# Performance work log

Measured on AMD Instinct MI355X. Metric: run time of the kernel, lower is better.

## Reference

```python
import jax, jax.numpy as jnp
import numpy as np

B = 512; S = 6; Q = 2            # meta-batch, n_way*k_shot, n_way*q_query
DIM = 64; IMG = 28; N_WAY = 2
HEADS = 4; HD = DIM // HEADS     # retrieval heads / head dim
EPS = 1e-5


def _pool_mat(inp, out):
    # exact torch AdaptiveAvgPool2d windowing as a matrix [out, inp]
    P = np.zeros((out, inp), np.float32)
    for i in range(out):
        s = (i * inp) // out
        e = -((-(i + 1) * inp) // out)
        P[i, s:e] = 1.0 / (e - s)
    return jnp.asarray(P)

P28 = _pool_mat(IMG, 8)  # 28 -> 8; subsequent 8 -> 8 pools are identity


def _gelu(x):
    return jax.nn.gelu(x, approximate=False)


def _conv(x, w, b):
    y = jax.lax.conv_general_dilated(x, w, (1, 1), ((1, 1), (1, 1)),
                                     dimension_numbers=('NCHW', 'OIHW', 'NCHW'))
    return y + b[None, :, None, None]


def _bn(x, p):
    # p rows: gamma, beta, running_mean, running_var (eval-mode BatchNorm2d)
    g, bt, m, v = p[0], p[1], p[2], p[3]
    sc = g / jnp.sqrt(v + EPS)
    return (x - m[None, :, None, None]) * sc[None, :, None, None] + bt[None, :, None, None]


def _img_in(x, c1w, c1b, bn1, c2w, c2b, bn2, c3w, c3b, bn3, c4w, c4b, bn4, lin_w):
    h = _bn(_conv(x, c1w, c1b), bn1)
    h = jnp.einsum('oi,ncij,pj->ncop', P28, h, P28)   # adaptive avg pool 28x28 -> 8x8
    h = _gelu(h)                                       # dropout is identity in eval
    h = _gelu(_bn(_conv(h, c2w, c2b), bn2))
    h = _gelu(_bn(_conv(h, c3w, c3b), bn3))
    h = _gelu(_bn(_conv(h, c4w, c4b), bn4))            # -> [N,1,8,8]
    h = h.reshape(h.shape[0], -1)                      # [N,64]
    return h @ lin_w.T                                 # Linear(64 -> DIM, no bias)


def _net(x, w1, w2):
    # x: [B,K,D]; w1,w2: [B,D,D] batched fast weights
    h = jnp.einsum('bed,bkd->bke', w1, x)
    ah = _gelu(h)
    y = jnp.einsum('bed,bkd->bke', w2, ah)
    return y, h


def _get_lor(x, w1, w2, r_q, r_k, r_v, r_o, ln_w, ln_b):
    b, k, _ = x.shape
    q, _ = _net(x, w1, w2)
    qh = jnp.einsum('nhd,bkd->bknh', r_q, q)
    sc = jnp.einsum('bknh,rnh->bknr', qh, r_k) / (HD ** 0.5)
    p = jax.nn.softmax(sc, axis=-1)
    lor = jnp.einsum('bknr,rnh->bknh', p, r_v).reshape(b, k, DIM)
    lor = jnp.einsum('de,bkd->bke', r_o, lor)
    z = lor + x
    mu = z.mean(-1, keepdims=True)
    var = ((z - mu) ** 2).mean(-1, keepdims=True)
    return (z - mu) / jnp.sqrt(var + EPS) * ln_w + ln_b


def _forward(query_w, sxs, qxs, inner_lr, c1w, c1b, bn1, c2w, c2b, bn2, c3w, c3b, bn3,
             c4w, c4b, bn4, lin_w, emb, w1, w2, tags, r_q, r_k, r_v, r_o, ln_w, ln_b,
             sys, qys):
    b = query_w.shape[0]
    s = sxs.shape[1]
    q = qxs.shape[1]
    feats = lambda im: _img_in(im.reshape(-1, 1, IMG, IMG), c1w, c1b, bn1, c2w, c2b,
                               bn2, c3w, c3b, bn3, c4w, c4b, bn4, lin_w)
    sx = feats(sxs).reshape(b, s, DIM)
    qx = feats(qxs).reshape(b, q, DIM)
    qe = tags[4]
    w1b = jnp.broadcast_to(w1, (b, DIM, DIM))
    w2b = jnp.broadcast_to(w2, (b, DIM, DIM))
    bound = sx + emb[sys]                                          # [B,S,D]
    # all 4 tag variants for all S shots in one vectorized get_lor call
    inp = (bound[:, :, None, :] + tags[:4][None, None]).reshape(b, s * 4, DIM)
    lors = _get_lor(inp, w1b, w2b, r_q, r_k, r_v, r_o, ln_w, ln_b).reshape(b, s, 4, DIM)
    l1s, r1s, l2s, r2s = lors[:, :, 0], lors[:, :, 1], lors[:, :, 2], lors[:, :, 3]
    qw1 = w1[None] + jnp.einsum('bsl,bsr->blr', l1s, r1s)
    qw2 = w2[None] + jnp.einsum('bsl,bsr->blr', l2s, r2s)
    preds, _ = _net(qx + qe, qw1, qw2)                             # [B,Q,D]
    logits = jnp.einsum('ld,bqd->bql', emb, preds).reshape(-1, N_WAY)
    labels = qys.reshape(-1)
    ls = jax.nn.log_softmax(logits)
    task_loss = -jnp.take_along_axis(ls, labels[:, None], axis=1).mean()
    n_correct = (jnp.argmax(logits, axis=1) == labels).sum()
    return task_loss, n_correct, b * q


def setup_inputs() -> dict:
    key = jax.random.key(0)
    ks = jax.random.split(key, 24)
    rn = lambda i, sh, sc=1.0: sc * jax.random.normal(ks[i], sh, jnp.float32)
    def bnp(i, c):
        k0, k1, k2 = jax.random.split(ks[i], 3)
        return jnp.stack([1.0 + 0.1 * jax.random.normal(k0, (c,)),
                          0.1 * jax.random.normal(k1, (c,)),
                          0.1 * jax.random.normal(k2, (c,)),
                          0.5 + jax.random.uniform(jax.random.fold_in(ks[i], 3), (c,))])
    return {
        'query_w': rn(0, (B, DIM)),
        'sxs': rn(1, (B, S, IMG * IMG)),
        'qxs': rn(2, (B, Q, IMG * IMG)),
        'inner_lr': jnp.float32(0.1),
        'c1w': rn(3, (32, 1, 3, 3), 0.3), 'c1b': rn(4, (32,), 0.1), 'bn1': bnp(5, 32),
        'c2w': rn(6, (32, 32, 3, 3), 0.06), 'c2b': rn(7, (32,), 0.1), 'bn2': bnp(8, 32),
        'c3w': rn(9, (32, 32, 3, 3), 0.06), 'c3b': rn(10, (32,), 0.1), 'bn3': bnp(11, 32),
        'c4w': rn(12, (1, 32, 3, 3), 0.06), 'c4b': rn(13, (1,), 0.1), 'bn4': bnp(14, 1),
        'lin_w': rn(15, (DIM, 64), 0.125),
        'emb': rn(16, (N_WAY, DIM), 0.125),
        'w1': rn(17, (DIM, DIM), 0.125),
        'w2': rn(18, (DIM, DIM), 0.125),
        'tags': rn(19, (8, DIM), 0.125),
        'r_q': rn(20, (HEADS, HD, DIM), 0.125),
        'r_k': rn(21, (16, HEADS, HD), 0.25),
        'r_v': rn(22, (16, HEADS, HD), 0.25),
        'r_o': rn(23, (DIM, DIM), 0.125),
        'ln_w': 0.001 * jnp.ones((DIM,), jnp.float32),
        'ln_b': jnp.zeros((DIM,), jnp.float32),
        'sys': jax.random.randint(jax.random.fold_in(key, 100), (B, S), 0, N_WAY),
        'qys': jax.random.randint(jax.random.fold_in(key, 101), (B, Q), 0, N_WAY),
    }


def reference(query_w, sxs, qxs, inner_lr, c1w, c1b, bn1, c2w, c2b, bn2, c3w, c3b, bn3,
              c4w, c4b, bn4, lin_w, emb, w1, w2, tags, r_q, r_k, r_v, r_o, ln_w, ln_b,
              sys, qys):
    task_loss, n_correct, n_q = _forward(query_w, sxs, qxs, inner_lr, c1w, c1b, bn1,
                                         c2w, c2b, bn2, c3w, c3b, bn3, c4w, c4b, bn4,
                                         lin_w, emb, w1, w2, tags, r_q, r_k, r_v, r_o,
                                         ln_w, ln_b, sys, qys)
    return (task_loss, task_loss, jnp.float32(0.0), n_correct, n_q)
```

## Files before the change

kernel.cpp:

```cpp
#include <hip/hip_runtime.h>
#include <math.h>

constexpr int NSUP = 3072;
constexpr float EPSF = 1e-5f;

constexpr int WS_W1B  = 0;
constexpr int WS_B1   = 1024;
constexpr int WS_W2B  = 1056;
constexpr int WS_W3B  = 5664;
constexpr int WS_W4B  = 10272;
constexpr int WS_B4   = 10416;
constexpr int WS_B2   = 10420;
constexpr int WS_B3   = 10452;
constexpr int WS_HW1  = 10484;
constexpr int WS_HW2  = 12788;
constexpr int WS_HRQ  = 15092;
constexpr int WS_HROT = 17396;
constexpr int WS_PART = 19700;
constexpr int WS_FEATS= 20724;

using short8 = __attribute__((ext_vector_type(8))) short;
using f32x4  = __attribute__((ext_vector_type(4))) float;

__device__ __forceinline__ float gelu_f(float x) {
    float z  = fabsf(x) * 0.70710678118654752440f;
    float t  = __builtin_amdgcn_rcpf(__builtin_fmaf(0.3275911f, z, 1.0f));
    float p  = t * __builtin_fmaf(t,
                 __builtin_fmaf(t,
                   __builtin_fmaf(t,
                     __builtin_fmaf(t, 1.061405429f, -1.453152027f),
                     1.421413741f),
                   -0.284496736f),
                 0.254829592f);
    float e  = __expf(-z * z);
    float er = __builtin_fmaf(-p, e, 1.0f);
    float s  = copysignf(er, x);
    return 0.5f * x * (1.0f + s);
}
__device__ __forceinline__ unsigned short f2bf(float f) {
    unsigned u = __float_as_uint(f);
    return (unsigned short)((u + 0x7FFFu + ((u >> 16) & 1u)) >> 16);
}
__device__ __forceinline__ float bflo(unsigned u) { return __uint_as_float(u << 16); }
__device__ __forceinline__ float bfhi(unsigned u) { return __uint_as_float(u & 0xffff0000u); }

__global__ void __launch_bounds__(256) precompute_kernel(
    const float* __restrict__ c1w, const float* __restrict__ c1b, const float* __restrict__ bn1,
    const float* __restrict__ c2w, const float* __restrict__ c2b, const float* __restrict__ bn2,
    const float* __restrict__ c3w, const float* __restrict__ c3b, const float* __restrict__ bn3,
    const float* __restrict__ c4w, const float* __restrict__ c4b, const float* __restrict__ bn4,
    const float* __restrict__ w1, const float* __restrict__ w2,
    const float* __restrict__ rq, const float* __restrict__ ro,
    float* __restrict__ ws)
{
    const int gid = blockIdx.x * 256 + threadIdx.x;
    const int gsz = gridDim.x * 256;

    unsigned short* w1b = (unsigned short*)(ws + WS_W1B);
    for (int v = gid; v < 2048; v += gsz) {
        int kt = v >> 10, rem = v & 1023, oc = rem >> 5, kk = rem & 31;
        int tap = kt * 32 + kk;
        unsigned short o = 0;
        if (tap < 36) {
            int tt = tap / 6, s = tap - tt * 6;
            float sum = 0.f;
            for (int di = 0; di < 3; ++di) {
                int a = tt - di; if (a < 0 || a > 3) continue;
                for (int dj = 0; dj < 3; ++dj) {
                    int bb = s - dj; if (bb < 0 || bb > 3) continue;
                    sum += c1w[oc * 9 + di * 3 + dj];
                }
            }
            float sc1 = bn1[oc] * rsqrtf(bn1[96 + oc] + EPSF);
            o = f2bf(sum * sc1 * (1.0f / 16.0f));
        }
        w1b[v] = o;
    }
    for (int c = gid; c < 32; c += gsz) {
        float sc1 = bn1[c] * rsqrtf(bn1[96 + c] + EPSF);
        ws[WS_B1 + c] = (c1b[c] - bn1[64 + c]) * sc1 + bn1[32 + c];
        float sc2 = bn2[c] * rsqrtf(bn2[96 + c] + EPSF);
        ws[WS_B2 + c] = (c2b[c] - bn2[64 + c]) * sc2 + bn2[32 + c];
        float sc3 = bn3[c] * rsqrtf(bn3[96 + c] + EPSF);
        ws[WS_B3 + c] = (c3b[c] - bn3[64 + c]) * sc3 + bn3[32 + c];
    }
    unsigned short* w2b = (unsigned short*)(ws + WS_W2B);
    unsigned short* w3b = (unsigned short*)(ws + WS_W3B);
    for (int v = gid; v < 9216; v += gsz) {
        int tap = v >> 10, oc = (v >> 5) & 31, ic = v & 31;
        float sc2 = bn2[oc] * rsqrtf(bn2[96 + oc] + EPSF);
        float sc3 = bn3[oc] * rsqrtf(bn3[96 + oc] + EPSF);
        w2b[v] = f2bf(c2w[oc * 288 + ic * 9 + tap] * sc2);
        w3b[v] = f2bf(c3w[oc * 288 + ic * 9 + tap] * sc3);
    }
    {
        unsigned short* w4b = (unsigned short*)(ws + WS_W4B);
        float sc4 = bn4[0] * rsqrtf(bn4[3] + EPSF);
        for (int v = gid; v < 288; v += gsz) {
            int tap = v >> 5, ic = v & 31;
            w4b[v] = f2bf(c4w[ic * 9 + tap] * sc4);
        }
        if (gid == 0) ws[WS_B4] = (c4b[0] - bn4[2]) * sc4 + bn4[1];
    }
    unsigned short* hw1 = (unsigned short*)(ws + WS_HW1);
    unsigned short* hw2 = (unsigned short*)(ws + WS_HW2);
    unsigned short* hrq = (unsigned short*)(ws + WS_HRQ);
    unsigned short* hro = (unsigned short*)(ws + WS_HROT);
    for (int v = gid; v < 4608; v += gsz) {
        int e = v / 72, d = v - e * 72;
        unsigned short a = 0, b = 0, c = 0, r = 0;
        if (d < 64) {
            a = f2bf(w1[e * 64 + d]);
            b = f2bf(w2[e * 64 + d]);
            c = f2bf(rq[e * 64 + d]);
            r = f2bf(ro[d * 64 + e]);
        }
        hw1[v] = a; hw2[v] = b; hrq[v] = c; hro[v] = r;
    }
}

__device__ __forceinline__ void conv32(unsigned short* __restrict__ A,
                                       const unsigned short* __restrict__ W,
                                       float bi0, float bi1, int col, int quad)
{
    f32x4 acc[4][2];
    #pragma unroll
    for (int mt = 0; mt < 4; ++mt) { acc[mt][0] = (f32x4){0,0,0,0}; acc[mt][1] = (f32x4){0,0,0,0}; }
    const unsigned short* abase[4];
    #pragma unroll
    for (int mt = 0; mt < 4; ++mt) {
        int px = mt * 16 + col;
        abase[mt] = A + ((px >> 3) * 10 + (px & 7)) * 32 + quad * 8;
    }
    #pragma unroll
    for (int dr = 0; dr < 3; ++dr)
        #pragma unroll
        for (int dc = 0; dc < 3; ++dc) {
            int tap = dr * 3 + dc;
            short8 b0 = *(const short8*)(W + (tap * 32 + col) * 32 + quad * 8);
            short8 b1 = *(const short8*)(W + (tap * 32 + 16 + col) * 32 + quad * 8);
            #pragma unroll
            for (int mt = 0; mt < 4; ++mt) {
                short8 a = *(const short8*)(abase[mt] + (dr * 10 + dc) * 32);
                acc[mt][0] = __builtin_amdgcn_mfma_f32_16x16x32_bf16(a, b0, acc[mt][0], 0, 0, 0);
                acc[mt][1] = __builtin_amdgcn_mfma_f32_16x16x32_bf16(a, b1, acc[mt][1], 0, 0, 0);
            }
        }
    #pragma unroll
    for (int mt = 0; mt < 4; ++mt)
        #pragma unroll
        for (int reg = 0; reg < 4; ++reg) {
            int px = mt * 16 + quad * 4 + reg;
            unsigned short* dst = A + (((px >> 3) + 1) * 10 + (px & 7) + 1) * 32;
            dst[col]      = f2bf(gelu_f(acc[mt][0][reg] + bi0));
            dst[col + 16] = f2bf(gelu_f(acc[mt][1][reg] + bi1));
        }
}

__global__ void __launch_bounds__(512, 4) feats_kernel(
    const float* __restrict__ sxs, const float* __restrict__ qxs,
    const float* __restrict__ lin_w, const float* __restrict__ ws,
    float* __restrict__ feats)
{
    __shared__ __align__(16) unsigned short sAct[8][3200];
    __shared__ __align__(16) unsigned short sWB[9216];
    __shared__ __align__(16) unsigned short sW4[288];
    __shared__ __align__(16) float sh4[8][64];

    const int t    = threadIdx.x;
    const int wv   = t >> 6;
    const int lane = t & 63;
    const int col  = lane & 15;
    const int quad = lane >> 4;
    const int n    = blockIdx.x * 8 + wv;

    unsigned short* A = sAct[wv];

    const uint4* w2v = (const uint4*)(ws + WS_W2B);
    uint4 pw0 = w2v[t];
    uint4 pw1 = w2v[t + 512];
    uint4 pw2 = {0, 0, 0, 0};
    if (t < 128) pw2 = w2v[t + 1024];

    {
        const float* img = (n < NSUP) ? (sxs + (size_t)n * 784) : (qxs + (size_t)(n - NSUP) * 784);
        const float4* sv = (const float4*)img;
        #pragma unroll
        for (int j = 0; j < 4; ++j) {
            int idx = j * 64 + lane;
            if (idx < 196) {
                float4 v = sv[idx];
                ushort4 o = { f2bf(v.x), f2bf(v.y), f2bf(v.z), f2bf(v.w) };
                *(ushort4*)(A + idx * 4) = o;
            }
        }
    }
    if (t < 256) ((uint4*)sWB)[t] = ((const uint4*)(ws + WS_W1B))[t];
    __syncthreads();

    {
        int ttj[8], ssj[8];
        #pragma unroll
        for (int j = 0; j < 8; ++j) {
            int k = quad * 8 + j;
            ttj[j] = k / 6; ssj[j] = k - ttj[j] * 6;
        }
        f32x4 acc[4][2];
        #pragma unroll
        for (int mt = 0; mt < 4; ++mt) { acc[mt][0] = (f32x4){0,0,0,0}; acc[mt][1] = (f32x4){0,0,0,0}; }

        short8 b00 = *(const short8*)(sWB + (0 * 32 + 0 * 16 + col) * 32 + quad * 8);
        short8 b01 = *(const short8*)(sWB + (0 * 32 + 1 * 16 + col) * 32 + quad * 8);
        short8 b10 = *(const short8*)(sWB + (1 * 32 + 0 * 16 + col) * 32 + quad * 8);
        short8 b11 = *(const short8*)(sWB + (1 * 32 + 1 * 16 + col) * 32 + quad * 8);

        #pragma unroll
        for (int mt = 0; mt < 4; ++mt) {
            int px = mt * 16 + col;
            int sr = (((px >> 3) * 7) >> 1) - 1;
            int sc = (((px & 7) * 7) >> 1) - 1;
            short8 a0;
            #pragma unroll
            for (int j = 0; j < 8; ++j) {
                int rr = sr + ttj[j], cc = sc + ssj[j];
                bool ok = ((unsigned)rr < 28u) && ((unsigned)cc < 28u);
                int off = ok ? (rr * 28 + cc) : 0;
                unsigned short hv = A[off];
                a0[j] = ok ? (short)hv : (short)0;
            }
            acc[mt][0] = __builtin_amdgcn_mfma_f32_16x16x32_bf16(a0, b00, acc[mt][0], 0, 0, 0);
            acc[mt][1] = __builtin_amdgcn_mfma_f32_16x16x32_bf16(a0, b01, acc[mt][1], 0, 0, 0);
            short8 a1 = {0,0,0,0,0,0,0,0};
            if (quad == 0) {
                #pragma unroll
                for (int j = 0; j < 4; ++j) {
                    int rr = sr + 5, cc = sc + 2 + j;
                    bool ok = ((unsigned)rr < 28u) && ((unsigned)cc < 28u);
                    int off = ok ? (rr * 28 + cc) : 0;
                    unsigned short hv = A[off];
                    a1[j] = ok ? (short)hv : (short)0;
                }
            }
            acc[mt][0] = __builtin_amdgcn_mfma_f32_16x16x32_bf16(a1, b10, acc[mt][0], 0, 0, 0);
            acc[mt][1] = __builtin_amdgcn_mfma_f32_16x16x32_bf16(a1, b11, acc[mt][1], 0, 0, 0);
        }

        {
            uint4 z4 = {0, 0, 0, 0};
            #pragma unroll
            for (int it = 0; it < 3; ++it) {
                int h = lane + it * 64;
                if (h < 144) {
                    int u4;
                    if (h < 40)      u4 = h;
                    else if (h < 80) u4 = 360 + (h - 40);
                    else {
                        int k = h - 80; int r = 1 + (k >> 3); int cj = k & 7;
                        u4 = r * 40 + ((cj >= 4) ? (32 + cj) : cj);
                    }
                    ((uint4*)A)[u4] = z4;
                }
            }
        }
        float bi0 = ws[WS_B1 + col], bi1 = ws[WS_B1 + 16 + col];
        #pragma unroll
        for (int mt = 0; mt < 4; ++mt)
            #pragma unroll
            for (int reg = 0; reg < 4; ++reg) {
                int px = mt * 16 + quad * 4 + reg;
                unsigned short* dst = A + (((px >> 3) + 1) * 10 + (px & 7) + 1) * 32;
                dst[col]      = f2bf(gelu_f(acc[mt][0][reg] + bi0));
                dst[col + 16] = f2bf(gelu_f(acc[mt][1][reg] + bi1));
            }
    }
    __syncthreads();

    {
        ((uint4*)sWB)[t]       = pw0;
        ((uint4*)sWB)[t + 512] = pw1;
        if (t < 128) ((uint4*)sWB)[t + 1024] = pw2;
        if (t < 36)  ((uint4*)sW4)[t] = ((const uint4*)(ws + WS_W4B))[t];
        const uint4* w3v = (const uint4*)(ws + WS_W3B);
        pw0 = w3v[t];
        pw1 = w3v[t + 512];
        if (t < 128) pw2 = w3v[t + 1024];
    }
    __syncthreads();

    conv32(A, sWB, ws[WS_B2 + col], ws[WS_B2 + 16 + col], col, quad);
    __syncthreads();
    {
        ((uint4*)sWB)[t]       = pw0;
        ((uint4*)sWB)[t + 512] = pw1;
        if (t < 128) ((uint4*)sWB)[t + 1024] = pw2;
    }
    __syncthreads();
    conv32(A, sWB, ws[WS_B3 + col], ws[WS_B3 + 16 + col], col, quad);

    {
        f32x4 acc4[4];
        #pragma unroll
        for (int mt = 0; mt < 4; ++mt) acc4[mt] = (f32x4){0,0,0,0};
        const unsigned short* abase[4];
        #pragma unroll
        for (int mt = 0; mt < 4; ++mt) {
            int px = mt * 16 + col;
            abase[mt] = A + ((px >> 3) * 10 + (px & 7)) * 32 + quad * 8;
        }
        #pragma unroll
        for (int dr = 0; dr < 3; ++dr)
            #pragma unroll
            for (int dc = 0; dc < 3; ++dc) {
                int tap = dr * 3 + dc;
                short8 b = *(const short8*)(sW4 + tap * 32 + quad * 8);
                #pragma unroll
                for (int mt = 0; mt < 4; ++mt) {
                    short8 a = *(const short8*)(abase[mt] + (dr * 10 + dc) * 32);
                    acc4[mt] = __builtin_amdgcn_mfma_f32_16x16x32_bf16(a, b, acc4[mt], 0, 0, 0);
                }
            }
        if (col < 4) {
            f32x4 v = acc4[0];
            if (col == 1) v = acc4[1];
            else if (col == 2) v = acc4[2];
            else if (col == 3) v = acc4[3];
            float b4 = ws[WS_B4];
            #pragma unroll
            for (int reg = 0; reg < 4; ++reg)
                sh4[wv][col * 16 + quad * 4 + reg] = gelu_f(v[reg] + b4);
        }
    }

    {
        const float4* lw = (const float4*)(lin_w + (size_t)lane * 64);
        const float4* hp = (const float4*)sh4[wv];
        float acc = 0.f;
        #pragma unroll
        for (int j = 0; j < 16; ++j) {
            float4 w = lw[j], h = hp[j];
            acc += w.x * h.x + w.y * h.y + w.z * h.z + w.w * h.w;
        }
        feats[n * 64 + lane] = acc;
    }
}

__device__ __forceinline__ void head_gemm(const unsigned short* __restrict__ Ab,
                                          const unsigned short* __restrict__ Bw,
                                          int col, int quad, int wvid, f32x4 res[2])
{
    #pragma unroll
    for (int u = 0; u < 2; ++u) {
        int tau = wvid + u * 4;
        int mt = tau & 1, nt = tau >> 1;
        f32x4 acc = {0, 0, 0, 0};
        #pragma unroll
        for (int kt = 0; kt < 2; ++kt) {
            short8 a = *(const short8*)(Ab + (mt * 16 + col) * 72 + kt * 32 + quad * 8);
            short8 b = *(const short8*)(Bw + (nt * 16 + col) * 72 + kt * 32 + quad * 8);
            acc = __builtin_amdgcn_mfma_f32_16x16x32_bf16(a, b, acc, 0, 0, 0);
        }
        res[u] = acc;
    }
}

__global__ void __launch_bounds__(256, 2) head_kernel(
    const float* __restrict__ emb, const float* __restrict__ tags,
    const float* __restrict__ rk, const float* __restrict__ rv,
    const float* __restrict__ lnw, const float* __restrict__ lnb,
    const int* __restrict__ sys, const int* __restrict__ qys,
    const float* __restrict__ ws, const float* __restrict__ feats,
    float* __restrict__ part)
{
    __shared__ __align__(16) unsigned short sW1B[4608], sW2B[4608], sRQB[4608], sROT[4608];
    __shared__ __align__(16) unsigned short bufA[2304], bufB[2304];
    __shared__ __align__(16) float sXf[1536];
    __shared__ __align__(16) float sRK[1024], sRV[1024];
    __shared__ __align__(16) float s_xq[128], s_ah[128], s_yp[128];
    __shared__ float s_t1[12], s_t2[12], s_mu[24], s_rs[24], s_lg[4];

    const int t    = threadIdx.x;
    const int b    = blockIdx.x;
    const int wvid = t >> 6;
    const int col  = t & 15;
    const int quad = (t >> 4) & 3;

    ((float4*)sRK)[t] = ((const float4*)rk)[t];
    ((float4*)sRV)[t] = ((const float4*)rv)[t];
    for (int i = t; i < 576; i += 256) {
        ((uint4*)sW1B)[i] = ((const uint4*)(ws + WS_HW1))[i];
        ((uint4*)sW2B)[i] = ((const uint4*)(ws + WS_HW2))[i];
        ((uint4*)sRQB)[i] = ((const uint4*)(ws + WS_HRQ))[i];
        ((uint4*)sROT)[i] = ((const uint4*)(ws + WS_HROT))[i];
    }
    if (t < 72) {
        uint4 z = {0, 0, 0, 0};
        ((uint4*)(bufA + 1728))[t] = z;
        ((uint4*)(bufB + 1728))[t] = z;
    }
    for (int idx = t; idx < 1536; idx += 256) {
        int k = idx >> 6, e = idx & 63;
        int s = k >> 2, tg = k & 3;
        int cls = sys[b * 6 + s];
        float v = feats[(b * 6 + s) * 64 + e] + emb[cls * 64 + e] + tags[tg * 64 + e];
        sXf[idx] = v;
        bufA[k * 72 + e] = f2bf(v);
    }
    __syncthreads();

    f32x4 r[2];
    head_gemm(bufA, sW1B, col, quad, wvid, r);
    #pragma unroll
    for (int u = 0; u < 2; ++u) {
        int tau = wvid + u * 4, mt = tau & 1, nt = tau >> 1;
        #pragma unroll
        for (int reg = 0; reg < 4; ++reg) {
            int row = mt * 16 + quad * 4 + reg;
            if (row < 24) bufB[row * 72 + nt * 16 + col] = f2bf(gelu_f(r[u][reg]));
        }
    }
    __syncthreads();
    head_gemm(bufB, sW2B, col, quad, wvid, r);
    #pragma unroll
    for (int u = 0; u < 2; ++u) {
        int tau = wvid + u * 4, mt = tau & 1, nt = tau >> 1;
        #pragma unroll
        for (int reg = 0; reg < 4; ++reg) {
            int row = mt * 16 + quad * 4 + reg;
            if (row < 24) bufA[row * 72 + nt * 16 + col] = f2bf(r[u][reg]);
        }
    }
    __syncthreads();
    head_gemm(bufA, sRQB, col, quad, wvid, r);
    #pragma unroll
    for (int u = 0; u < 2; ++u) {
        int tau = wvid + u * 4, mt = tau & 1, nt = tau >> 1;
        #pragma unroll
        for (int reg = 0; reg < 4; ++reg) {
            int row = mt * 16 + quad * 4 + reg;
            if (row < 24) bufB[row * 72 + nt * 16 + col] = f2bf(r[u][reg]);
        }
    }
    __syncthreads();

    if (t < 96) {
        int k = t >> 2, nn = t & 3;
        const unsigned short* qp = bufB + k * 72 + nn * 16;
        uint4 u0 = *(const uint4*)(qp);
        uint4 u1 = *(const uint4*)(qp + 8);
        float qv[16];
        qv[0]=bflo(u0.x); qv[1]=bfhi(u0.x); qv[2]=bflo(u0.y); qv[3]=bfhi(u0.y);
        qv[4]=bflo(u0.z); qv[5]=bfhi(u0.z); qv[6]=bflo(u0.w); qv[7]=bfhi(u0.w);
        qv[8]=bflo(u1.x); qv[9]=bfhi(u1.x); qv[10]=bflo(u1.y); qv[11]=bfhi(u1.y);
        qv[12]=bflo(u1.z); qv[13]=bfhi(u1.z); qv[14]=bflo(u1.w); qv[15]=bfhi(u1.w);
        float sc[16]; float mx = -1e30f;
        #pragma unroll
        for (int rr = 0; rr < 16; ++rr) {
            const float* kp = sRK + rr * 64 + nn * 16;
            float d = 0.f;
            #pragma unroll
            for (int h = 0; h < 16; ++h) d += qv[h] * kp[h];
            d *= 0.25f;
            sc[rr] = d; mx = fmaxf(mx, d);
        }
        float sum = 0.f;
        #pragma unroll
        for (int rr = 0; rr < 16; ++rr) { sc[rr] = __expf(sc[rr] - mx); sum += sc[rr]; }
        float inv = 1.0f / sum;
        float o[16];
        #pragma unroll
        for (int h = 0; h < 16; ++h) o[h] = 0.f;
        #pragma unroll
        for (int rr = 0; rr < 16; ++rr) {
            const float* vp = sRV + rr * 64 + nn * 16;
            float p = sc[rr];
            #pragma unroll
            for (int h = 0; h < 16; ++h) o[h] += p * vp[h];
        }
        unsigned short* op = bufA + k * 72 + nn * 16;
        #pragma unroll
        for (int h = 0; h < 16; ++h) op[h] = f2bf(o[h] * inv);
    }
    __syncthreads();

    head_gemm(bufA, sROT, col, quad, wvid, r);
    #pragma unroll
    for (int u = 0; u < 2; ++u) {
        int tau = wvid + u * 4, mt = tau & 1, nt = tau >> 1;
        #pragma unroll
        for (int reg = 0; reg < 4; ++reg) {
            int row = mt * 16 + quad * 4 + reg;
            if (row < 24) {
                int idx = row * 64 + nt * 16 + col;
                sXf[idx] = sXf[idx] + r[u][reg];
            }
        }
    }
    __syncthreads();

    if (t < 24) {
        const float4* zp = (const float4*)(sXf + t * 64);
        float sx_ = 0.f;
        #pragma unroll
        for (int j = 0; j < 16; ++j) {
            float4 v = zp[(j + t) & 15];
            sx_ += v.x + v.y + v.z + v.w;
        }
        float mu = sx_ * (1.0f / 64.0f);
        float vv = 0.f;
        #pragma unroll
        for (int j = 0; j < 16; ++j) {
            float4 v = zp[(j + t) & 15];
            float d0 = v.x - mu, d1 = v.y - mu, d2 = v.z - mu, d3 = v.w - mu;
            vv += d0*d0 + d1*d1 + d2*d2 + d3*d3;
        }
        s_mu[t] = mu;
        s_rs[t] = 1.0f / sqrtf(vv * (1.0f / 64.0f) + EPSF);
    }
    __syncthreads();
    for (int idx = t; idx < 1536; idx += 256) {
        int k = idx >> 6, e = idx & 63;
        float v = (sXf[idx] - s_mu[k]) * s_rs[k] * lnw[e] + lnb[e];
        bufB[k * 72 + e] = f2bf(v);
    }
    if (t < 128) {
        int q = t >> 6, e = t & 63;
        s_xq[t] = feats[(NSUP + b * 2 + q) * 64 + e] + tags[256 + e];
    }
    __syncthreads();

    if (t < 12) {
        int q = t / 6, s = t - q * 6;
        const uint4* rp = (const uint4*)(bufB + (s * 4 + 1) * 72);
        const float* xp = s_xq + q * 64;
        float d = 0.f;
        #pragma unroll
        for (int j = 0; j < 8; ++j) {
            uint4 u = rp[j];
            const float* x = xp + j * 8;
            d += bflo(u.x)*x[0] + bfhi(u.x)*x[1] + bflo(u.y)*x[2] + bfhi(u.y)*x[3]
               + bflo(u.z)*x[4] + bfhi(u.z)*x[5] + bflo(u.w)*x[6] + bfhi(u.w)*x[7];
        }
        s_t1[t] = d;
    }
    __syncthreads();
    if (t < 128) {
        int q = t >> 6, e = t & 63;
        const uint4* wp = (const uint4*)(sW1B + e * 72);
        const float* xp = s_xq + q * 64;
        float acc = 0.f;
        #pragma unroll
        for (int j = 0; j < 8; ++j) {
            uint4 u = wp[j];
            const float* x = xp + j * 8;
            acc += bflo(u.x)*x[0] + bfhi(u.x)*x[1] + bflo(u.y)*x[2] + bfhi(u.y)*x[3]
                 + bflo(u.z)*x[4] + bfhi(u.z)*x[5] + bflo(u.w)*x[6] + bfhi(u.w)*x[7];
        }
        #pragma unroll
        for (int s = 0; s < 6; ++s)
            acc += bflo((unsigned)bufB[(s * 4 + 0) * 72 + e]) * s_t1[q * 6 + s];
        s_ah[t] = gelu_f(acc);
    }
    __syncthreads();
    if (t < 12) {
        int q = t / 6, s = t - q * 6;
        const uint4* rp = (const uint4*)(bufB + (s * 4 + 3) * 72);
        const float* xp = s_ah + q * 64;
        float d = 0.f;
        #pragma unroll
        for (int j = 0; j < 8; ++j) {
            uint4 u = rp[j];
            const float* x = xp + j * 8;
            d += bflo(u.x)*x[0] + bfhi(u.x)*x[1] + bflo(u.y)*x[2] + bfhi(u.y)*x[3]
               + bflo(u.z)*x[4] + bfhi(u.z)*x[5] + bflo(u.w)*x[6] + bfhi(u.w)*x[7];
        }
        s_t2[t] = d;
    }
    __syncthreads();
    if (t < 128) {
        int q = t >> 6, e = t & 63;
        const uint4* wp = (const uint4*)(sW2B + e * 72);
        const float* xp = s_ah + q * 64;
        float acc = 0.f;
        #pragma unroll
        for (int j = 0; j < 8; ++j) {
            uint4 u = wp[j];
            const float* x = xp + j * 8;
            acc += bflo(u.x)*x[0] + bfhi(u.x)*x[1] + bflo(u.y)*x[2] + bfhi(u.y)*x[3]
                 + bflo(u.z)*x[4] + bfhi(u.z)*x[5] + bflo(u.w)*x[6] + bfhi(u.w)*x[7];
        }
        #pragma unroll
        for (int s = 0; s < 6; ++s)
            acc += bflo((unsigned)bufB[(s * 4 + 2) * 72 + e]) * s_t2[q * 6 + s];
        s_yp[t] = acc;
    }
    __syncthreads();
    if (t < 4) {
        int q = t >> 1, ll = t & 1;
        const float4* ep = (const float4*)(emb + ll * 64);
        const float4* yp = (const float4*)(s_yp + q * 64);
        float d = 0.f;
        #pragma unroll
        for (int j = 0; j < 16; ++j) {
            float4 a = ep[j], x = yp[j];
            d += a.x*x.x + a.y*x.y + a.z*x.z + a.w*x.w;
        }
        s_lg[t] = d;
    }
    __syncthreads();
    if (t == 0) {
        float lsum = 0.f, corr = 0.f;
        #pragma unroll
        for (int q = 0; q < 2; ++q) {
            float l0 = s_lg[q * 2], l1 = s_lg[q * 2 + 1];
            int lab = qys[b * 2 + q];
            float m = fmaxf(l0, l1);
            float lse = m + logf(expf(l0 - m) + expf(l1 - m));
            lsum += -((lab ? l1 : l0) - lse);
            int pred = (l1 > l0) ? 1 : 0;
            corr += (pred == lab) ? 1.0f : 0.0f;
        }
        part[b] = lsum;
        part[512 + b] = corr;
    }
}

__global__ void __launch_bounds__(256) finalize_kernel(const float* __restrict__ part,
                                                       float* __restrict__ out)
{
    __shared__ float sl[256], sc[256];
    const int t = threadIdx.x;
    sl[t] = part[t] + part[t + 256];
    sc[t] = part[512 + t] + part[768 + t];
    __syncthreads();
    for (int s = 128; s > 0; s >>= 1) {
        if (t < s) { sl[t] += sl[t + s]; sc[t] += sc[t + s]; }
        __syncthreads();
    }
    if (t == 0) {
        float loss = sl[0] * (1.0f / 1024.0f);
        out[0] = loss;
        out[1] = loss;
        out[2] = 0.0f;
        out[3] = sc[0];
        out[4] = 1024.0f;
    }
}

extern "C" void kernel_launch(void* const* d_in, const int* in_sizes, int n_in,
                              void* d_out, int out_size, void* d_ws, size_t ws_size,
                              hipStream_t stream)
{
    (void)in_sizes; (void)n_in; (void)out_size; (void)ws_size;
    const float* sxs  = (const float*)d_in[1];
    const float* qxs  = (const float*)d_in[2];
    const float* c1w  = (const float*)d_in[4];
    const float* c1b  = (const float*)d_in[5];
    const float* bn1  = (const float*)d_in[6];
    const float* c2w  = (const float*)d_in[7];
    const float* c2b  = (const float*)d_in[8];
    const float* bn2  = (const float*)d_in[9];
    const float* c3w  = (const float*)d_in[10];
    const float* c3b  = (const float*)d_in[11];
    const float* bn3  = (const float*)d_in[12];
    const float* c4w  = (const float*)d_in[13];
    const float* c4b  = (const float*)d_in[14];
    const float* bn4  = (const float*)d_in[15];
    const float* lin_w= (const float*)d_in[16];
    const float* emb  = (const float*)d_in[17];
    const float* w1   = (const float*)d_in[18];
    const float* w2   = (const float*)d_in[19];
    const float* tags = (const float*)d_in[20];
    const float* rq   = (const float*)d_in[21];
    const float* rk   = (const float*)d_in[22];
    const float* rv   = (const float*)d_in[23];
    const float* ro   = (const float*)d_in[24];
    const float* lnw  = (const float*)d_in[25];
    const float* lnb  = (const float*)d_in[26];
    const int*   sys  = (const int*)d_in[27];
    const int*   qys  = (const int*)d_in[28];

    float* ws  = (float*)d_ws;
    float* out = (float*)d_out;

    precompute_kernel<<<64, 256, 0, stream>>>(c1w, c1b, bn1, c2w, c2b, bn2,
                                              c3w, c3b, bn3, c4w, c4b, bn4,
                                              w1, w2, rq, ro, ws);
    feats_kernel<<<512, 512, 0, stream>>>(sxs, qxs, lin_w, ws, ws + WS_FEATS);
    head_kernel<<<512, 256, 0, stream>>>(emb, tags, rk, rv, lnw, lnb, sys, qys,
                                         ws, ws + WS_FEATS, ws + WS_PART);
    finalize_kernel<<<1, 256, 0, stream>>>(ws + WS_PART, out);
}
```

Measured before the change: 168.7 us.

## Split each image's convs across two waves and reorder LDS layouts for MFMA

```diff
diff --git a/kernel.cpp b/kernel.cpp
--- a/kernel.cpp
+++ b/kernel.cpp
@@ -58,8 +58,9 @@
 
     unsigned short* w1b = (unsigned short*)(ws + WS_W1B);
     for (int v = gid; v < 2048; v += gsz) {
-        int kt = v >> 10, rem = v & 1023, oc = rem >> 5, kk = rem & 31;
-        int tap = kt * 32 + kk;
+        int c8 = v & 7, colx = (v >> 3) & 15, qd = (v >> 7) & 3, hh = (v >> 9) & 1, kt = v >> 10;
+        int tap = kt * 32 + qd * 8 + c8;
+        int oc = hh * 16 + colx;
         unsigned short o = 0;
         if (tap < 36) {
             int tt = tap / 6, s = tap - tt * 6;
@@ -87,7 +88,9 @@
     unsigned short* w2b = (unsigned short*)(ws + WS_W2B);
     unsigned short* w3b = (unsigned short*)(ws + WS_W3B);
     for (int v = gid; v < 9216; v += gsz) {
-        int tap = v >> 10, oc = (v >> 5) & 31, ic = v & 31;
+        int c8 = v & 7, colx = (v >> 3) & 15, qd = (v >> 7) & 3, hh = (v >> 9) & 1, tap = v >> 10;
+        int oc = hh * 16 + colx;
+        int ic = qd * 8 + c8;
         float sc2 = bn2[oc] * rsqrtf(bn2[96 + oc] + EPSF);
         float sc3 = bn3[oc] * rsqrtf(bn3[96 + oc] + EPSF);
         w2b[v] = f2bf(c2w[oc * 288 + ic * 9 + tap] * sc2);
@@ -119,45 +122,51 @@
     }
 }
 
-__device__ __forceinline__ void conv32(unsigned short* __restrict__ A,
-                                       const unsigned short* __restrict__ W,
-                                       float bi0, float bi1, int col, int quad)
-{
-    f32x4 acc[4][2];
-    #pragma unroll
-    for (int mt = 0; mt < 4; ++mt) { acc[mt][0] = (f32x4){0,0,0,0}; acc[mt][1] = (f32x4){0,0,0,0}; }
-    const unsigned short* abase[4];
-    #pragma unroll
-    for (int mt = 0; mt < 4; ++mt) {
-        int px = mt * 16 + col;
-        abase[mt] = A + ((px >> 3) * 10 + (px & 7)) * 32 + quad * 8;
+__device__ __forceinline__ void conv32_mfma(const unsigned short* __restrict__ A,
+                                            const unsigned short* __restrict__ W,
+                                            int col, int quad, int half,
+                                            f32x4 (&acc)[2][2])
+{
+    int ab[2];
+    #pragma unroll
+    for (int m = 0; m < 2; ++m) {
+        int px = (half * 2 + m) * 16 + col;
+        ab[m] = quad * 800 + ((px >> 3) * 10 + (px & 7)) * 8;
+        acc[m][0] = (f32x4){0,0,0,0};
+        acc[m][1] = (f32x4){0,0,0,0};
     }
     #pragma unroll
     for (int dr = 0; dr < 3; ++dr)
         #pragma unroll
         for (int dc = 0; dc < 3; ++dc) {
             int tap = dr * 3 + dc;
-            short8 b0 = *(const short8*)(W + (tap * 32 + col) * 32 + quad * 8);
-            short8 b1 = *(const short8*)(W + (tap * 32 + 16 + col) * 32 + quad * 8);
+            short8 b0 = *(const short8*)(W + (((tap * 2 + 0) * 4 + quad) * 16 + col) * 8);
+            short8 b1 = *(const short8*)(W + (((tap * 2 + 1) * 4 + quad) * 16 + col) * 8);
             #pragma unroll
-            for (int mt = 0; mt < 4; ++mt) {
-                short8 a = *(const short8*)(abase[mt] + (dr * 10 + dc) * 32);
-                acc[mt][0] = __builtin_amdgcn_mfma_f32_16x16x32_bf16(a, b0, acc[mt][0], 0, 0, 0);
-                acc[mt][1] = __builtin_amdgcn_mfma_f32_16x16x32_bf16(a, b1, acc[mt][1], 0, 0, 0);
-            }
-        }
-    #pragma unroll
-    for (int mt = 0; mt < 4; ++mt)
+            for (int m = 0; m < 2; ++m) {
+                short8 a = *(const short8*)(A + ab[m] + (dr * 10 + dc) * 8);
+                acc[m][0] = __builtin_amdgcn_mfma_f32_16x16x32_bf16(a, b0, acc[m][0], 0, 0, 0);
+                acc[m][1] = __builtin_amdgcn_mfma_f32_16x16x32_bf16(a, b1, acc[m][1], 0, 0, 0);
+            }
+        }
+}
+
+__device__ __forceinline__ void conv_store(unsigned short* __restrict__ A,
+                                           const f32x4 (&acc)[2][2],
+                                           float bi0, float bi1, int col, int quad, int half)
+{
+    #pragma unroll
+    for (int m = 0; m < 2; ++m)
         #pragma unroll
         for (int reg = 0; reg < 4; ++reg) {
-            int px = mt * 16 + quad * 4 + reg;
-            unsigned short* dst = A + (((px >> 3) + 1) * 10 + (px & 7) + 1) * 32;
-            dst[col]      = f2bf(gelu_f(acc[mt][0][reg] + bi0));
-            dst[col + 16] = f2bf(gelu_f(acc[mt][1][reg] + bi1));
-        }
-}
-
-__global__ void __launch_bounds__(512, 4) feats_kernel(
+            int px = (half * 2 + m) * 16 + quad * 4 + reg;
+            int P = ((px >> 3) + 1) * 10 + (px & 7) + 1;
+            A[(col >> 3) * 800 + P * 8 + (col & 7)]       = f2bf(gelu_f(acc[m][0][reg] + bi0));
+            A[(2 + (col >> 3)) * 800 + P * 8 + (col & 7)] = f2bf(gelu_f(acc[m][1][reg] + bi1));
+        }
+}
+
+__global__ void __launch_bounds__(1024, 8) feats_kernel(
     const float* __restrict__ sxs, const float* __restrict__ qxs,
     const float* __restrict__ lin_w, const float* __restrict__ ws,
     float* __restrict__ feats)
@@ -169,25 +178,31 @@
 
     const int t    = threadIdx.x;
     const int wv   = t >> 6;
+    const int half = wv & 1;
+    const int iw   = wv >> 1;
     const int lane = t & 63;
     const int col  = lane & 15;
     const int quad = lane >> 4;
-    const int n    = blockIdx.x * 8 + wv;
-
-    unsigned short* A = sAct[wv];
+    const int n    = blockIdx.x * 8 + iw;
+
+    unsigned short* A = sAct[iw];
+
+    float bi1a = ws[WS_B1 + col],      bi1b = ws[WS_B1 + 16 + col];
+    float bi2a = ws[WS_B2 + col],      bi2b = ws[WS_B2 + 16 + col];
+    float bi3a = ws[WS_B3 + col],      bi3b = ws[WS_B3 + 16 + col];
+    float b4   = ws[WS_B4];
 
     const uint4* w2v = (const uint4*)(ws + WS_W2B);
-    uint4 pw0 = w2v[t];
-    uint4 pw1 = w2v[t + 512];
-    uint4 pw2 = {0, 0, 0, 0};
-    if (t < 128) pw2 = w2v[t + 1024];
+    uint4 pwA = w2v[t];
+    uint4 pwB = {0, 0, 0, 0};
+    if (t < 128) pwB = w2v[t + 1024];
 
     {
         const float* img = (n < NSUP) ? (sxs + (size_t)n * 784) : (qxs + (size_t)(n - NSUP) * 784);
         const float4* sv = (const float4*)img;
         #pragma unroll
-        for (int j = 0; j < 4; ++j) {
-            int idx = j * 64 + lane;
+        for (int j = 0; j < 2; ++j) {
+            int idx = j * 128 + half * 64 + lane;
             if (idx < 196) {
                 float4 v = sv[idx];
                 ushort4 o = { f2bf(v.x), f2bf(v.y), f2bf(v.z), f2bf(v.w) };
@@ -198,6 +213,7 @@
     if (t < 256) ((uint4*)sWB)[t] = ((const uint4*)(ws + WS_W1B))[t];
     __syncthreads();
 
+    f32x4 acc[2][2];
     {
         int ttj[8], ssj[8];
         #pragma unroll
@@ -205,18 +221,16 @@
             int k = quad * 8 + j;
             ttj[j] = k / 6; ssj[j] = k - ttj[j] * 6;
         }
-        f32x4 acc[4][2];
-        #pragma unroll
-        for (int mt = 0; mt < 4; ++mt) { acc[mt][0] = (f32x4){0,0,0,0}; acc[mt][1] = (f32x4){0,0,0,0}; }
-
-        short8 b00 = *(const short8*)(sWB + (0 * 32 + 0 * 16 + col) * 32 + quad * 8);
-        short8 b01 = *(const short8*)(sWB + (0 * 32 + 1 * 16 + col) * 32 + quad * 8);
-        short8 b10 = *(const short8*)(sWB + (1 * 32 + 0 * 16 + col) * 32 + quad * 8);
-        short8 b11 = *(const short8*)(sWB + (1 * 32 + 1 * 16 + col) * 32 + quad * 8);
-
-        #pragma unroll
-        for (int mt = 0; mt < 4; ++mt) {
-            int px = mt * 16 + col;
+        short8 b00 = *(const short8*)(sWB + ((0 * 4 + quad) * 16 + col) * 8);
+        short8 b01 = *(const short8*)(sWB + ((1 * 4 + quad) * 16 + col) * 8);
+        short8 b10 = *(const short8*)(sWB + ((2 * 4 + quad) * 16 + col) * 8);
+        short8 b11 = *(const short8*)(sWB + ((3 * 4 + quad) * 16 + col) * 8);
+
+        #pragma unroll
+        for (int m = 0; m < 2; ++m) {
+            acc[m][0] = (f32x4){0,0,0,0};
+            acc[m][1] = (f32x4){0,0,0,0};
+            int px = (half * 2 + m) * 16 + col;
             int sr = (((px >> 3) * 7) >> 1) - 1;
             int sc = (((px & 7) * 7) >> 1) - 1;
             short8 a0;
@@ -228,8 +242,8 @@
                 unsigned short hv = A[off];
                 a0[j] = ok ? (short)hv : (short)0;
             }
-            acc[mt][0] = __builtin_amdgcn_mfma_f32_16x16x32_bf16(a0, b00, acc[mt][0], 0, 0, 0);
-            acc[mt][1] = __builtin_amdgcn_mfma_f32_16x16x32_bf16(a0, b01, acc[mt][1], 0, 0, 0);
+            acc[m][0] = __builtin_amdgcn_mfma_f32_16x16x32_bf16(a0, b00, acc[m][0], 0, 0, 0);
+            acc[m][1] = __builtin_amdgcn_mfma_f32_16x16x32_bf16(a0, b01, acc[m][1], 0, 0, 0);
             short8 a1 = {0,0,0,0,0,0,0,0};
             if (quad == 0) {
                 #pragma unroll
@@ -241,71 +255,58 @@
                     a1[j] = ok ? (short)hv : (short)0;
                 }
             }
-            acc[mt][0] = __builtin_amdgcn_mfma_f32_16x16x32_bf16(a1, b10, acc[mt][0], 0, 0, 0);
-            acc[mt][1] = __builtin_amdgcn_mfma_f32_16x16x32_bf16(a1, b11, acc[mt][1], 0, 0, 0);
-        }
-
-        {
-            uint4 z4 = {0, 0, 0, 0};
-            #pragma unroll
-            for (int it = 0; it < 3; ++it) {
-                int h = lane + it * 64;
-                if (h < 144) {
-                    int u4;
-                    if (h < 40)      u4 = h;
-                    else if (h < 80) u4 = 360 + (h - 40);
-                    else {
-                        int k = h - 80; int r = 1 + (k >> 3); int cj = k & 7;
-                        u4 = r * 40 + ((cj >= 4) ? (32 + cj) : cj);
-                    }
-                    ((uint4*)A)[u4] = z4;
-                }
-            }
-        }
-        float bi0 = ws[WS_B1 + col], bi1 = ws[WS_B1 + 16 + col];
-        #pragma unroll
-        for (int mt = 0; mt < 4; ++mt)
-            #pragma unroll
-            for (int reg = 0; reg < 4; ++reg) {
-                int px = mt * 16 + quad * 4 + reg;
-                unsigned short* dst = A + (((px >> 3) + 1) * 10 + (px & 7) + 1) * 32;
-                dst[col]      = f2bf(gelu_f(acc[mt][0][reg] + bi0));
-                dst[col + 16] = f2bf(gelu_f(acc[mt][1][reg] + bi1));
-            }
+            acc[m][0] = __builtin_amdgcn_mfma_f32_16x16x32_bf16(a1, b10, acc[m][0], 0, 0, 0);
+            acc[m][1] = __builtin_amdgcn_mfma_f32_16x16x32_bf16(a1, b11, acc[m][1], 0, 0, 0);
+        }
     }
     __syncthreads();
 
     {
-        ((uint4*)sWB)[t]       = pw0;
-        ((uint4*)sWB)[t + 512] = pw1;
-        if (t < 128) ((uint4*)sWB)[t + 1024] = pw2;
+        uint4 z4 = {0, 0, 0, 0};
+        int t2 = half * 64 + lane;
+        #pragma unroll
+        for (int it = 0; it < 2; ++it) {
+            int h = t2 + it * 128;
+            if (h < 144) {
+                int pi = h >> 2, ch = h & 3;
+                int P;
+                if (pi < 10)      P = pi;
+                else if (pi < 20) P = 90 + (pi - 10);
+                else { int r = 1 + ((pi - 20) >> 1); P = r * 10 + ((pi - 20) & 1) * 9; }
+                ((uint4*)A)[ch * 100 + P] = z4;
+            }
+        }
+        conv_store(A, acc, bi1a, bi1b, col, quad, half);
+
+        ((uint4*)sWB)[t] = pwA;
+        if (t < 128) ((uint4*)sWB)[t + 1024] = pwB;
         if (t < 36)  ((uint4*)sW4)[t] = ((const uint4*)(ws + WS_W4B))[t];
         const uint4* w3v = (const uint4*)(ws + WS_W3B);
-        pw0 = w3v[t];
-        pw1 = w3v[t + 512];
-        if (t < 128) pw2 = w3v[t + 1024];
-    }
-    __syncthreads();
-
-    conv32(A, sWB, ws[WS_B2 + col], ws[WS_B2 + 16 + col], col, quad);
-    __syncthreads();
+        pwA = w3v[t];
+        if (t < 128) pwB = w3v[t + 1024];
+    }
+    __syncthreads();
+
+    conv32_mfma(A, sWB, col, quad, half, acc);
+    __syncthreads();
+    conv_store(A, acc, bi2a, bi2b, col, quad, half);
+    ((uint4*)sWB)[t] = pwA;
+    if (t < 128) ((uint4*)sWB)[t + 1024] = pwB;
+    __syncthreads();
+
+    conv32_mfma(A, sWB, col, quad, half, acc);
+    __syncthreads();
+    conv_store(A, acc, bi3a, bi3b, col, quad, half);
+    __syncthreads();
+
     {
-        ((uint4*)sWB)[t]       = pw0;
-        ((uint4*)sWB)[t + 512] = pw1;
-        if (t < 128) ((uint4*)sWB)[t + 1024] = pw2;
-    }
-    __syncthreads();
-    conv32(A, sWB, ws[WS_B3 + col], ws[WS_B3 + 16 + col], col, quad);
-
-    {
-        f32x4 acc4[4];
-        #pragma unroll
-        for (int mt = 0; mt < 4; ++mt) acc4[mt] = (f32x4){0,0,0,0};
-        const unsigned short* abase[4];
-        #pragma unroll
-        for (int mt = 0; mt < 4; ++mt) {
-            int px = mt * 16 + col;
-            abase[mt] = A + ((px >> 3) * 10 + (px & 7)) * 32 + quad * 8;
+        f32x4 acc4[2];
+        int ab[2];
+        #pragma unroll
+        for (int m = 0; m < 2; ++m) {
+            int px = (half * 2 + m) * 16 + col;
+            ab[m] = quad * 800 + ((px >> 3) * 10 + (px & 7)) * 8;
+            acc4[m] = (f32x4){0,0,0,0};
         }
         #pragma unroll
         for (int dr = 0; dr < 3; ++dr)
@@ -314,33 +315,31 @@
                 int tap = dr * 3 + dc;
                 short8 b = *(const short8*)(sW4 + tap * 32 + quad * 8);
                 #pragma unroll
-                for (int mt = 0; mt < 4; ++mt) {
-                    short8 a = *(const short8*)(abase[mt] + (dr * 10 + dc) * 32);
-                    acc4[mt] = __builtin_amdgcn_mfma_f32_16x16x32_bf16(a, b, acc4[mt], 0, 0, 0);
+                for (int m = 0; m < 2; ++m) {
+                    short8 a = *(const short8*)(A + ab[m] + (dr * 10 + dc) * 8);
+                    acc4[m] = __builtin_amdgcn_mfma_f32_16x16x32_bf16(a, b, acc4[m], 0, 0, 0);
                 }
             }
-        if (col < 4) {
-            f32x4 v = acc4[0];
-            if (col == 1) v = acc4[1];
-            else if (col == 2) v = acc4[2];
-            else if (col == 3) v = acc4[3];
-            float b4 = ws[WS_B4];
+        if (col < 2) {
+            f32x4 v = (col == 0) ? acc4[0] : acc4[1];
             #pragma unroll
             for (int reg = 0; reg < 4; ++reg)
-                sh4[wv][col * 16 + quad * 4 + reg] = gelu_f(v[reg] + b4);
-        }
-    }
+                sh4[iw][(half * 2 + col) * 16 + quad * 4 + reg] = gelu_f(v[reg] + b4);
+        }
+    }
+    __syncthreads();
 
     {
-        const float4* lw = (const float4*)(lin_w + (size_t)lane * 64);
-        const float4* hp = (const float4*)sh4[wv];
-        float acc = 0.f;
+        int o = half * 32 + (lane & 31);
+        const float4* lw = (const float4*)(lin_w + (size_t)o * 64);
+        const float4* hp = (const float4*)sh4[iw];
+        float acc2 = 0.f;
         #pragma unroll
         for (int j = 0; j < 16; ++j) {
             float4 w = lw[j], h = hp[j];
-            acc += w.x * h.x + w.y * h.y + w.z * h.z + w.w * h.w;
-        }
-        feats[n * 64 + lane] = acc;
+            acc2 += w.x * h.x + w.y * h.y + w.z * h.z + w.w * h.w;
+        }
+        if (lane < 32) feats[n * 64 + o] = acc2;
     }
 }
 
@@ -685,7 +684,7 @@
     precompute_kernel<<<64, 256, 0, stream>>>(c1w, c1b, bn1, c2w, c2b, bn2,
                                               c3w, c3b, bn3, c4w, c4b, bn4,
                                               w1, w2, rq, ro, ws);
-    feats_kernel<<<512, 512, 0, stream>>>(sxs, qxs, lin_w, ws, ws + WS_FEATS);
+    feats_kernel<<<512, 1024, 0, stream>>>(sxs, qxs, lin_w, ws, ws + WS_FEATS);
     head_kernel<<<512, 256, 0, stream>>>(emb, tags, rk, rv, lnw, lnb, sys, qys,
                                          ws, ws + WS_FEATS, ws + WS_PART);
     finalize_kernel<<<1, 256, 0, stream>>>(ws + WS_PART, out);
```

Result: slower. 187.2 us (+10.9%).
